# Kernel tuning notes

Measured on AMD Instinct MI355X. Metric: run time of the kernel, lower is better.

## Reference

```python
import jax, jax.numpy as jnp
import numpy as np

N = 16384
NUM_EMB = 8192
D = 512
K_SEL = 4
COMMIT = 0.25


def setup_inputs() -> dict:
    key = jax.random.key(0)
    k1, k2 = jax.random.split(key)
    z_e = jax.random.normal(k1, (N, D), dtype=jnp.float32)
    # torch init: uniform(-1/num_embeddings, 1/num_embeddings)
    lim = 1.0 / NUM_EMB
    codebook = jax.random.uniform(k2, (NUM_EMB, D), dtype=jnp.float32,
                                  minval=-lim, maxval=lim)
    return {"z_e": z_e, "codebook": codebook, "k": K_SEL}


def reference(z_e, codebook, k):
    # distances: ||z||^2 - 2 z.W^T + ||w||^2  -> [N, NUM_EMB]
    distances = (jnp.sum(z_e * z_e, axis=1, keepdims=True)
                 - 2.0 * jnp.matmul(z_e, codebook.T)
                 + jnp.sum(codebook * codebook, axis=1))
    # top-k smallest distances
    _, indices = jax.lax.top_k(-distances, k)  # [N, k]
    n = z_e.shape[0]
    k_hot = jnp.zeros((n, codebook.shape[0]), dtype=z_e.dtype)
    k_hot = k_hot.at[jnp.arange(n)[:, None], indices].set(1.0)
    quantized_k = codebook[indices]            # [N, k, D]
    z_q = quantized_k.mean(axis=1)             # [N, D]
    codebook_loss = jnp.mean((z_q - jax.lax.stop_gradient(z_e)) ** 2)
    commitment_loss = COMMIT * jnp.mean((z_e - jax.lax.stop_gradient(z_q)) ** 2)
    vq_loss = codebook_loss + commitment_loss
    z_q_ste = z_e + jax.lax.stop_gradient(z_q - z_e)  # straight-through
    return (z_q_ste, vq_loss, k_hot)
```

## Files before the change

### kernel.cpp

```cpp
#include <hip/hip_runtime.h>

#define N_ROWS 16384
#define N_EMB  8192
#define DIM    512
#define NCAND  16


typedef short  bhalf8  __attribute__((ext_vector_type(8)));
typedef float  floatx4 __attribute__((ext_vector_type(4)));

__device__ __forceinline__ unsigned short f2b(float f) {
    unsigned u = __builtin_bit_cast(unsigned, f);
    unsigned r = (u + 0x7fffu + ((u >> 16) & 1u)) >> 16;
    return (unsigned short)r;
}
__device__ __forceinline__ unsigned pk2(float a, float b) {
    return (unsigned)f2b(a) | ((unsigned)f2b(b) << 16);
}

__global__ void convert_bf16_kernel(const float* __restrict__ ze,
                                    const float* __restrict__ cb,
                                    unsigned short* __restrict__ ze16,
                                    unsigned short* __restrict__ cb16) {
    size_t id = (size_t)blockIdx.x * 256 + threadIdx.x;
    const size_t nze = (size_t)N_ROWS * DIM / 8;
    const float* src;
    unsigned short* dst;
    size_t off;
    if (id < nze) { src = ze; dst = ze16; off = id * 8; }
    else          { src = cb; dst = cb16; off = (id - nze) * 8; }
    float4 a = *(const float4*)(src + off);
    float4 b = *(const float4*)(src + off + 4);
    uint4 u = { pk2(a.x, a.y), pk2(a.z, a.w), pk2(b.x, b.y), pk2(b.z, b.w) };
    *(uint4*)(dst + off) = u;
}

__launch_bounds__(256, 2)
__global__ void score_gemm_kernel(const unsigned short* __restrict__ ze16,
                                  const unsigned short* __restrict__ cb16,
                                  unsigned short* __restrict__ skeys) {
    __shared__ unsigned short As[128][40];
    __shared__ unsigned short Bs[128][40];

    const int t    = threadIdx.x;
    const int lane = t & 63;
    const int w    = t >> 6;
    const int rowBase = blockIdx.y * 128;
    const int colBase = blockIdx.x * 128;

    const int m  = lane & 15;
    const int q  = lane >> 4;
    const int wr = (w >> 1) * 64;
    const int wc = (w & 1) * 64;

    floatx4 acc[4][4];
    #pragma unroll
    for (int i = 0; i < 4; ++i)
        #pragma unroll
        for (int j = 0; j < 4; ++j)
            acc[i][j] = (floatx4){0.0f, 0.0f, 0.0f, 0.0f};

    const int sr = t >> 1;
    const int sk = (t & 1) * 16;
    const unsigned short* pa = ze16 + (size_t)(rowBase + sr) * DIM + sk;
    const unsigned short* pb = cb16 + (size_t)(colBase + sr) * DIM + sk;

    for (int k0 = 0; k0 < DIM; k0 += 32) {
        uint4 va0 = *(const uint4*)(pa + k0);
        uint4 va1 = *(const uint4*)(pa + k0 + 8);
        uint4 vb0 = *(const uint4*)(pb + k0);
        uint4 vb1 = *(const uint4*)(pb + k0 + 8);
        __syncthreads();
        *(uint4*)&As[sr][sk]     = va0;
        *(uint4*)&As[sr][sk + 8] = va1;
        *(uint4*)&Bs[sr][sk]     = vb0;
        *(uint4*)&Bs[sr][sk + 8] = vb1;
        __syncthreads();

        bhalf8 af[4], bf[4];
        #pragma unroll
        for (int i = 0; i < 4; ++i) af[i] = *(bhalf8*)&As[wr + i * 16 + m][q * 8];
        #pragma unroll
        for (int j = 0; j < 4; ++j) bf[j] = *(bhalf8*)&Bs[wc + j * 16 + m][q * 8];
        #pragma unroll
        for (int i = 0; i < 4; ++i)
            #pragma unroll
            for (int j = 0; j < 4; ++j)
                acc[i][j] = __builtin_amdgcn_mfma_f32_16x16x32_bf16(af[i], bf[j], acc[i][j], 0, 0, 0);
    }

    #pragma unroll
    for (int i = 0; i < 4; ++i) {
        #pragma unroll
        for (int reg = 0; reg < 4; ++reg) {
            int grow = rowBase + wr + i * 16 + q * 4 + reg;
            unsigned short* sp = skeys + (size_t)grow * N_EMB + colBase + wc + m;
            #pragma unroll
            for (int j = 0; j < 4; ++j) {
                unsigned short b = f2b(-acc[i][j][reg]);
                unsigned short s = (unsigned short)(b ^ ((b & 0x8000u) ? 0xFFFFu : 0x8000u));
                sp[j * 16] = s;
            }
        }
    }
}

__global__ void topk_scan_kernel(const unsigned short* __restrict__ skeys,
                                 int* __restrict__ cand) {
    const int wv   = threadIdx.x >> 6;
    const int lane = threadIdx.x & 63;
    const int row  = blockIdx.x * 4 + wv;
    const uint4* base = (const uint4*)(skeys + (size_t)row * N_EMB);

    unsigned k8[8];
    #pragma unroll
    for (int s = 0; s < 8; ++s) k8[s] = 0xFFFFFFFFu;

    auto ins = [&](unsigned e) {
        #pragma unroll
        for (int s = 0; s < 8; ++s) {
            unsigned lo = k8[s] < e ? k8[s] : e;
            unsigned hi = k8[s] < e ? e : k8[s];
            k8[s] = lo; e = hi;
        }
    };

    for (int it = 0; it < 16; ++it) {
        uint4 v = base[it * 64 + lane];
        unsigned colb = (unsigned)(it * 64 + lane) * 8;
        ins((v.x << 16) | (colb + 0)); ins((v.x & 0xFFFF0000u) | (colb + 1));
        ins((v.y << 16) | (colb + 2)); ins((v.y & 0xFFFF0000u) | (colb + 3));
        ins((v.z << 16) | (colb + 4)); ins((v.z & 0xFFFF0000u) | (colb + 5));
        ins((v.w << 16) | (colb + 6)); ins((v.w & 0xFFFF0000u) | (colb + 7));
    }

    unsigned win[NCAND];
    #pragma unroll
    for (int s = 0; s < NCAND; ++s) {
        unsigned mk = k8[0];
        #pragma unroll
        for (int d = 32; d; d >>= 1) {
            unsigned o = __shfl_xor(mk, d, 64);
            mk = o < mk ? o : mk;
        }
        win[s] = mk;
        bool pop = (k8[0] == mk);
        #pragma unroll
        for (int u = 0; u < 7; ++u) k8[u] = pop ? k8[u + 1] : k8[u];
        k8[7] = pop ? 0xFFFFFFFFu : k8[7];
    }

    if (lane == 0) {
        int* cp = cand + (size_t)row * NCAND;
        int4 o0 = { (int)(win[0] & 0xFFFFu),  (int)(win[1] & 0xFFFFu),
                    (int)(win[2] & 0xFFFFu),  (int)(win[3] & 0xFFFFu) };
        int4 o1 = { (int)(win[4] & 0xFFFFu),  (int)(win[5] & 0xFFFFu),
                    (int)(win[6] & 0xFFFFu),  (int)(win[7] & 0xFFFFu) };
        int4 o2 = { (int)(win[8] & 0xFFFFu),  (int)(win[9] & 0xFFFFu),
                    (int)(win[10] & 0xFFFFu), (int)(win[11] & 0xFFFFu) };
        int4 o3 = { (int)(win[12] & 0xFFFFu), (int)(win[13] & 0xFFFFu),
                    (int)(win[14] & 0xFFFFu), (int)(win[15] & 0xFFFFu) };
        *(int4*)(cp + 0)  = o0;
        *(int4*)(cp + 4)  = o1;
        *(int4*)(cp + 8)  = o2;
        *(int4*)(cp + 12) = o3;
    }
}

__global__ void rescore_kernel(const float* __restrict__ ze,
                               const float* __restrict__ cb,
                               const int* __restrict__ cand,
                               float* __restrict__ out_zq,
                               float* __restrict__ out_khot,
                               double* __restrict__ lossAcc) {
    __shared__ float zsh[4][DIM];
    const int wv = threadIdx.x >> 6;
    const int lane = threadIdx.x & 63;
    const int row = blockIdx.x * 4 + wv;

    {
        const float* zp = ze + (size_t)row * DIM + lane * 8;
        float4 v0 = *(const float4*)zp;
        float4 v1 = *(const float4*)(zp + 4);
        *(float4*)&zsh[wv][lane * 8]     = v0;
        *(float4*)&zsh[wv][lane * 8 + 4] = v1;
    }
    __syncthreads();

    float racc = 0.0f;
    {
        const int b = (lane >> 3) & 3;
        const int j = lane & 7;
        const float* zr = &zsh[wv][128 * b + j];
        #pragma unroll
        for (int i = 0; i < 16; ++i) {
            float zk = zr[8 * i];
            float sq = zk * zk;
            asm volatile("" : "+v"(sq));
            racc = racc + sq;
        }
    }
    float t1 = racc + __shfl_xor(racc, 1, 64);
    float t2 = t1 + __shfl_xor(t1, 2, 64);
    float t3 = t2 + __shfl_xor(t2, 4, 64);
    float zn = (__shfl(t3, 0, 64) + __shfl(t3, 8, 64))
             + (__shfl(t3, 16, 64) + __shfl(t3, 24, 64));

    float qv = 3.0e38f;
    int   idxv = 0x7fffffff;
    if (lane < NCAND) {
        idxv = cand[(size_t)row * NCAND + lane];
        const float* wp = cb + (size_t)idxv * DIM;
        const float* zz = zsh[wv];
        float acc1 = 0.0f;
        for (int k = 0; k < 384; k += 8) {
            float4 wa = *(const float4*)(wp + k);
            float4 wb = *(const float4*)(wp + k + 4);
            acc1 = __builtin_fmaf(zz[k + 0], wa.x, acc1);
            acc1 = __builtin_fmaf(zz[k + 1], wa.y, acc1);
            acc1 = __builtin_fmaf(zz[k + 2], wa.z, acc1);
            acc1 = __builtin_fmaf(zz[k + 3], wa.w, acc1);
            acc1 = __builtin_fmaf(zz[k + 4], wb.x, acc1);
            acc1 = __builtin_fmaf(zz[k + 5], wb.y, acc1);
            acc1 = __builtin_fmaf(zz[k + 6], wb.z, acc1);
            acc1 = __builtin_fmaf(zz[k + 7], wb.w, acc1);
        }
        float acc2 = 0.0f;
        for (int k = 384; k < 512; k += 8) {
            float4 wa = *(const float4*)(wp + k);
            float4 wb = *(const float4*)(wp + k + 4);
            acc2 = __builtin_fmaf(zz[k + 0], wa.x, acc2);
            acc2 = __builtin_fmaf(zz[k + 1], wa.y, acc2);
            acc2 = __builtin_fmaf(zz[k + 2], wa.z, acc2);
            acc2 = __builtin_fmaf(zz[k + 3], wa.w, acc2);
            acc2 = __builtin_fmaf(zz[k + 4], wb.x, acc2);
            acc2 = __builtin_fmaf(zz[k + 5], wb.y, acc2);
            acc2 = __builtin_fmaf(zz[k + 6], wb.z, acc2);
            acc2 = __builtin_fmaf(zz[k + 7], wb.w, acc2);
        }
        float Cv = acc1 + acc2;
        qv = zn - 2.0f * Cv;
    }

    float q[NCAND]; int id[NCAND];
    #pragma unroll
    for (int c = 0; c < NCAND; ++c) {
        q[c]  = __shfl(qv, c, 64);
        id[c] = __shfl(idxv, c, 64);
    }
    int selIdx[4];
    bool used[NCAND];
    #pragma unroll
    for (int c = 0; c < NCAND; ++c) used[c] = false;
    #pragma unroll
    for (int s = 0; s < 4; ++s) {
        float bq = 3.0e38f; int bi = 0x7fffffff; int bc = -1;
        #pragma unroll
        for (int c = 0; c < NCAND; ++c) {
            bool better = !used[c] && (q[c] < bq || (q[c] == bq && id[c] < bi));
            if (better) { bq = q[c]; bi = id[c]; bc = c; }
        }
        selIdx[s] = bi;
        #pragma unroll
        for (int c = 0; c < NCAND; ++c) used[c] = used[c] || (c == bc);
    }

    float zq[8] = { 0, 0, 0, 0, 0, 0, 0, 0 };
    #pragma unroll
    for (int s = 0; s < 4; ++s) {
        const float* wp = cb + (size_t)selIdx[s] * DIM + lane * 8;
        float4 w0 = *(const float4*)wp;
        float4 w1 = *(const float4*)(wp + 4);
        zq[0] += w0.x; zq[1] += w0.y; zq[2] += w0.z; zq[3] += w0.w;
        zq[4] += w1.x; zq[5] += w1.y; zq[6] += w1.z; zq[7] += w1.w;
    }

    float zf[8];
    {
        const float* zz = &zsh[wv][lane * 8];
        #pragma unroll
        for (int i = 0; i < 8; ++i) zf[i] = zz[i];
    }
    float o[8];
    double l = 0.0;
    #pragma unroll
    for (int i = 0; i < 8; ++i) {
        float zqf  = zq[i] * 0.25f;
        float diff = zqf - zf[i];
        o[i] = zf[i] + diff;
        double ld = (double)diff;
        l += ld * ld;
    }
    {
        float* op = out_zq + (size_t)row * DIM + lane * 8;
        float4 v0 = { o[0], o[1], o[2], o[3] };
        float4 v1 = { o[4], o[5], o[6], o[7] };
        *(float4*)op = v0;
        *(float4*)(op + 4) = v1;
    }
    #pragma unroll
    for (int mm = 32; mm; mm >>= 1) l += __shfl_xor(l, mm, 64);
    if (lane == 0) atomicAdd(lossAcc, l);

    if (lane < 4)
        out_khot[(size_t)row * N_EMB + selIdx[lane]] = 1.0f;
}

__global__ void finalize_kernel(const double* __restrict__ lossAcc,
                                float* __restrict__ out_loss) {
    if (threadIdx.x == 0 && blockIdx.x == 0)
        out_loss[0] = (float)(lossAcc[0] * (1.25 / ((double)N_ROWS * (double)DIM)));
}

extern "C" void kernel_launch(void* const* d_in, const int* in_sizes, int n_in,
                              void* d_out, int out_size, void* d_ws, size_t ws_size,
                              hipStream_t stream) {
    (void)in_sizes; (void)n_in; (void)out_size; (void)ws_size;
    const float* ze = (const float*)d_in[0];
    const float* cb = (const float*)d_in[1];

    float* out      = (float*)d_out;
    float* out_zq   = out;
    float* out_loss = out + (size_t)N_ROWS * DIM;
    float* out_khot = out_loss + 1;

    double* lossAcc = (double*)d_ws;
    int*    cand    = (int*)((char*)d_ws + 16);

    char* base = (char*)d_out;
    unsigned short* skeys = (unsigned short*)(base + 33554448);
    unsigned short* ze16  = (unsigned short*)(base + 33554448 + 268435456);
    unsigned short* cb16  = ze16 + (size_t)N_ROWS * DIM;

    hipMemsetAsync(lossAcc, 0, 16, stream);

    convert_bf16_kernel<<<6144, 256, 0, stream>>>(ze, cb, ze16, cb16);
    score_gemm_kernel<<<dim3(N_EMB / 128, N_ROWS / 128), 256, 0, stream>>>(ze16, cb16, skeys);
    topk_scan_kernel<<<N_ROWS / 4, 256, 0, stream>>>(skeys, cand);
    hipMemsetAsync(out_khot, 0, (size_t)N_ROWS * N_EMB * sizeof(float), stream);
    rescore_kernel<<<N_ROWS / 4, 256, 0, stream>>>(ze, cb, cand, out_zq, out_khot, lossAcc);
    finalize_kernel<<<1, 64, 0, stream>>>(lossAcc, out_loss);
}
```

Baseline: 1.170 ms.

## Fuse per-block top-8 selection into score GEMM epilogue, merge partial lists

The GEMM epilogue no longer writes the full bf16 score matrix. Each block now computes, per row, the top-8 keys over its 128 codebook columns using an in-register sorting network and a 16-lane shuffle reduction, then writes those to a small buffer. A new merge kernel reduces the 64 partial lists per row to 16 candidates. The aim is to remove the 256MB score write and re-read. In exchange the epilogue does more ALU work, the warp tiling changes to 2x8 MFMA tiles per wave, and launch bounds rise to 3 blocks per SM.

```diff
diff --git a/kernel.cpp b/kernel.cpp
--- a/kernel.cpp
+++ b/kernel.cpp
@@ -17,6 +17,12 @@
 __device__ __forceinline__ unsigned pk2(float a, float b) {
     return (unsigned)f2b(a) | ((unsigned)f2b(b) << 16);
 }
+__device__ __forceinline__ unsigned mkkey(float s, int col) {
+    unsigned short b = f2b(s);
+    unsigned short ts = (unsigned short)(b ^ ((b & 0x8000u) ? 0xFFFFu : 0x8000u));
+    return ((unsigned)ts << 16) | (unsigned)col;
+}
+__device__ __forceinline__ unsigned umn(unsigned a, unsigned b) { return a < b ? a : b; }
 
 __global__ void convert_bf16_kernel(const float* __restrict__ ze,
                                     const float* __restrict__ cb,
@@ -35,10 +41,10 @@
     *(uint4*)(dst + off) = u;
 }
 
-__launch_bounds__(256, 2)
-__global__ void score_gemm_kernel(const unsigned short* __restrict__ ze16,
-                                  const unsigned short* __restrict__ cb16,
-                                  unsigned short* __restrict__ skeys) {
+__launch_bounds__(256, 3)
+__global__ void score_gemm_topk_kernel(const unsigned short* __restrict__ ze16,
+                                       const unsigned short* __restrict__ cb16,
+                                       unsigned* __restrict__ blkTop) {
     __shared__ unsigned short As[128][40];
     __shared__ unsigned short Bs[128][40];
 
@@ -47,17 +53,16 @@
     const int w    = t >> 6;
     const int rowBase = blockIdx.y * 128;
     const int colBase = blockIdx.x * 128;
-
-    const int m  = lane & 15;
-    const int q  = lane >> 4;
-    const int wr = (w >> 1) * 64;
-    const int wc = (w & 1) * 64;
-
-    floatx4 acc[4][4];
-    #pragma unroll
-    for (int i = 0; i < 4; ++i)
-        #pragma unroll
-        for (int j = 0; j < 4; ++j)
+    const int cblk    = blockIdx.x;
+
+    const int m = lane & 15;
+    const int q = lane >> 4;
+
+    floatx4 acc[2][8];
+    #pragma unroll
+    for (int i = 0; i < 2; ++i)
+        #pragma unroll
+        for (int j = 0; j < 8; ++j)
             acc[i][j] = (floatx4){0.0f, 0.0f, 0.0f, 0.0f};
 
     const int sr = t >> 1;
@@ -77,94 +82,94 @@
         *(uint4*)&Bs[sr][sk + 8] = vb1;
         __syncthreads();
 
-        bhalf8 af[4], bf[4];
-        #pragma unroll
-        for (int i = 0; i < 4; ++i) af[i] = *(bhalf8*)&As[wr + i * 16 + m][q * 8];
-        #pragma unroll
-        for (int j = 0; j < 4; ++j) bf[j] = *(bhalf8*)&Bs[wc + j * 16 + m][q * 8];
-        #pragma unroll
-        for (int i = 0; i < 4; ++i)
+        bhalf8 af0 = *(bhalf8*)&As[w * 32 + m][q * 8];
+        bhalf8 af1 = *(bhalf8*)&As[w * 32 + 16 + m][q * 8];
+        #pragma unroll
+        for (int j = 0; j < 8; ++j) {
+            bhalf8 bf = *(bhalf8*)&Bs[j * 16 + m][q * 8];
+            acc[0][j] = __builtin_amdgcn_mfma_f32_16x16x32_bf16(af0, bf, acc[0][j], 0, 0, 0);
+            acc[1][j] = __builtin_amdgcn_mfma_f32_16x16x32_bf16(af1, bf, acc[1][j], 0, 0, 0);
+        }
+    }
+
+    #pragma unroll
+    for (int i = 0; i < 2; ++i) {
+        #pragma unroll
+        for (int reg = 0; reg < 4; ++reg) {
+            const int grow = rowBase + w * 32 + i * 16 + q * 4 + reg;
+            unsigned kk[8];
             #pragma unroll
-            for (int j = 0; j < 4; ++j)
-                acc[i][j] = __builtin_amdgcn_mfma_f32_16x16x32_bf16(af[i], bf[j], acc[i][j], 0, 0, 0);
-    }
-
-    #pragma unroll
-    for (int i = 0; i < 4; ++i) {
-        #pragma unroll
-        for (int reg = 0; reg < 4; ++reg) {
-            int grow = rowBase + wr + i * 16 + q * 4 + reg;
-            unsigned short* sp = skeys + (size_t)grow * N_EMB + colBase + wc + m;
+            for (int j = 0; j < 8; ++j) {
+                unsigned e = mkkey(-acc[i][j][reg], colBase + j * 16 + m);
+                kk[j] = e;
+                #pragma unroll
+                for (int s = 7; s > 0; --s) {
+                    if (s <= j) {
+                        unsigned lo = umn(kk[s - 1], kk[s]);
+                        unsigned hi = kk[s - 1] < kk[s] ? kk[s] : kk[s - 1];
+                        kk[s - 1] = lo; kk[s] = hi;
+                    }
+                }
+            }
+            unsigned sval = 0;
             #pragma unroll
-            for (int j = 0; j < 4; ++j) {
-                unsigned short b = f2b(-acc[i][j][reg]);
-                unsigned short s = (unsigned short)(b ^ ((b & 0x8000u) ? 0xFFFFu : 0x8000u));
-                sp[j * 16] = s;
+            for (int s = 0; s < 8; ++s) {
+                unsigned g = kk[0];
+                g = umn(g, (unsigned)__shfl_xor((int)g, 1, 64));
+                g = umn(g, (unsigned)__shfl_xor((int)g, 2, 64));
+                g = umn(g, (unsigned)__shfl_xor((int)g, 4, 64));
+                g = umn(g, (unsigned)__shfl_xor((int)g, 8, 64));
+                bool pop = (kk[0] == g);
+                #pragma unroll
+                for (int u = 0; u < 7; ++u) kk[u] = pop ? kk[u + 1] : kk[u];
+                kk[7] = pop ? 0xFFFFFFFFu : kk[7];
+                sval = (m == s) ? g : sval;
             }
-        }
-    }
-}
-
-__global__ void topk_scan_kernel(const unsigned short* __restrict__ skeys,
-                                 int* __restrict__ cand) {
+            if (m < 8)
+                blkTop[((size_t)grow * 64 + cblk) * 8 + m] = sval;
+        }
+    }
+}
+
+__global__ void merge_topk_kernel(const unsigned* __restrict__ blkTop,
+                                  int* __restrict__ cand) {
     const int wv   = threadIdx.x >> 6;
     const int lane = threadIdx.x & 63;
     const int row  = blockIdx.x * 4 + wv;
-    const uint4* base = (const uint4*)(skeys + (size_t)row * N_EMB);
-
-    unsigned k8[8];
-    #pragma unroll
-    for (int s = 0; s < 8; ++s) k8[s] = 0xFFFFFFFFu;
-
-    auto ins = [&](unsigned e) {
-        #pragma unroll
-        for (int s = 0; s < 8; ++s) {
-            unsigned lo = k8[s] < e ? k8[s] : e;
-            unsigned hi = k8[s] < e ? e : k8[s];
-            k8[s] = lo; e = hi;
-        }
-    };
-
-    for (int it = 0; it < 16; ++it) {
-        uint4 v = base[it * 64 + lane];
-        unsigned colb = (unsigned)(it * 64 + lane) * 8;
-        ins((v.x << 16) | (colb + 0)); ins((v.x & 0xFFFF0000u) | (colb + 1));
-        ins((v.y << 16) | (colb + 2)); ins((v.y & 0xFFFF0000u) | (colb + 3));
-        ins((v.z << 16) | (colb + 4)); ins((v.z & 0xFFFF0000u) | (colb + 5));
-        ins((v.w << 16) | (colb + 6)); ins((v.w & 0xFFFF0000u) | (colb + 7));
-    }
-
-    unsigned win[NCAND];
+    const uint4* base = (const uint4*)(blkTop + (size_t)row * 512);
+
+    uint4 a = base[lane * 2];
+    uint4 b = base[lane * 2 + 1];
+    unsigned in[8] = { a.x, a.y, a.z, a.w, b.x, b.y, b.z, b.w };
+    unsigned kk[8];
+    #pragma unroll
+    for (int j = 0; j < 8; ++j) {
+        kk[j] = in[j];
+        #pragma unroll
+        for (int s = 7; s > 0; --s) {
+            if (s <= j) {
+                unsigned lo = umn(kk[s - 1], kk[s]);
+                unsigned hi = kk[s - 1] < kk[s] ? kk[s] : kk[s - 1];
+                kk[s - 1] = lo; kk[s] = hi;
+            }
+        }
+    }
+
+    unsigned sval = 0;
     #pragma unroll
     for (int s = 0; s < NCAND; ++s) {
-        unsigned mk = k8[0];
-        #pragma unroll
-        for (int d = 32; d; d >>= 1) {
-            unsigned o = __shfl_xor(mk, d, 64);
-            mk = o < mk ? o : mk;
-        }
-        win[s] = mk;
-        bool pop = (k8[0] == mk);
-        #pragma unroll
-        for (int u = 0; u < 7; ++u) k8[u] = pop ? k8[u + 1] : k8[u];
-        k8[7] = pop ? 0xFFFFFFFFu : k8[7];
-    }
-
-    if (lane == 0) {
-        int* cp = cand + (size_t)row * NCAND;
-        int4 o0 = { (int)(win[0] & 0xFFFFu),  (int)(win[1] & 0xFFFFu),
-                    (int)(win[2] & 0xFFFFu),  (int)(win[3] & 0xFFFFu) };
-        int4 o1 = { (int)(win[4] & 0xFFFFu),  (int)(win[5] & 0xFFFFu),
-                    (int)(win[6] & 0xFFFFu),  (int)(win[7] & 0xFFFFu) };
-        int4 o2 = { (int)(win[8] & 0xFFFFu),  (int)(win[9] & 0xFFFFu),
-                    (int)(win[10] & 0xFFFFu), (int)(win[11] & 0xFFFFu) };
-        int4 o3 = { (int)(win[12] & 0xFFFFu), (int)(win[13] & 0xFFFFu),
-                    (int)(win[14] & 0xFFFFu), (int)(win[15] & 0xFFFFu) };
-        *(int4*)(cp + 0)  = o0;
-        *(int4*)(cp + 4)  = o1;
-        *(int4*)(cp + 8)  = o2;
-        *(int4*)(cp + 12) = o3;
-    }
+        unsigned g = kk[0];
+        #pragma unroll
+        for (int d = 32; d; d >>= 1)
+            g = umn(g, (unsigned)__shfl_xor((int)g, d, 64));
+        bool pop = (kk[0] == g);
+        #pragma unroll
+        for (int u = 0; u < 7; ++u) kk[u] = pop ? kk[u + 1] : kk[u];
+        kk[7] = pop ? 0xFFFFFFFFu : kk[7];
+        sval = (lane == s) ? g : sval;
+    }
+    if (lane < NCAND)
+        cand[(size_t)row * NCAND + lane] = (int)(sval & 0xFFFFu);
 }
 
 __global__ void rescore_kernel(const float* __restrict__ ze,
@@ -328,15 +333,15 @@
     int*    cand    = (int*)((char*)d_ws + 16);
 
     char* base = (char*)d_out;
-    unsigned short* skeys = (unsigned short*)(base + 33554448);
-    unsigned short* ze16  = (unsigned short*)(base + 33554448 + 268435456);
-    unsigned short* cb16  = ze16 + (size_t)N_ROWS * DIM;
+    unsigned*       blkTop = (unsigned*)(base + 33554448);
+    unsigned short* ze16   = (unsigned short*)(base + 33554448 + 33554432);
+    unsigned short* cb16   = ze16 + (size_t)N_ROWS * DIM;
 
     hipMemsetAsync(lossAcc, 0, 16, stream);
 
     convert_bf16_kernel<<<6144, 256, 0, stream>>>(ze, cb, ze16, cb16);
-    score_gemm_kernel<<<dim3(N_EMB / 128, N_ROWS / 128), 256, 0, stream>>>(ze16, cb16, skeys);
-    topk_scan_kernel<<<N_ROWS / 4, 256, 0, stream>>>(skeys, cand);
+    score_gemm_topk_kernel<<<dim3(N_EMB / 128, N_ROWS / 128), 256, 0, stream>>>(ze16, cb16, blkTop);
+    merge_topk_kernel<<<N_ROWS / 4, 256, 0, stream>>>(blkTop, cand);
     hipMemsetAsync(out_khot, 0, (size_t)N_ROWS * N_EMB * sizeof(float), stream);
     rescore_kernel<<<N_ROWS / 4, 256, 0, stream>>>(ze, cb, cand, out_zq, out_khot, lossAcc);
     finalize_kernel<<<1, 64, 0, stream>>>(lossAcc, out_loss);
```

Result: faster. 1.117 ms (-4.5%).
